# Optimization experiments

Hardware: AMD Instinct MI355X
Metric: run time of the kernel (lower is better)

The kernel has to match this reference:

```python
import jax, jax.numpy as jnp
import numpy as np

B, C, N, M_MODES, EMB = 8, 64, 2048, 32, 256
MFREQ = 2 * M_MODES * (2 * M_MODES - 1)  # 4032
SCALE = 1.0 / (C * C)


def setup_inputs() -> dict:
    key = jax.random.key(0)
    ks = jax.random.split(key, 16)
    d = {
        "x": jax.random.normal(ks[0], (B, C, N), jnp.float32),
        "emb": jax.random.normal(ks[1], (B, EMB), jnp.float32),
        "Vf_re": jax.random.normal(ks[2], (MFREQ, N), jnp.float32),
        "Vf_im": jax.random.normal(ks[3], (MFREQ, N), jnp.float32),
        "Vi_re": jax.random.normal(ks[4], (N, MFREQ), jnp.float32),
        "Vi_im": jax.random.normal(ks[5], (N, MFREQ), jnp.float32),
        "w1_re": SCALE * jax.random.uniform(ks[6], (C, C, M_MODES, M_MODES), jnp.float32),
        "w1_im": SCALE * jax.random.uniform(ks[7], (C, C, M_MODES, M_MODES), jnp.float32),
        "w2_re": SCALE * jax.random.uniform(ks[8], (C, C, M_MODES, M_MODES), jnp.float32),
        "w2_im": SCALE * jax.random.uniform(ks[9], (C, C, M_MODES, M_MODES), jnp.float32),
        "m1_re": SCALE * jax.random.uniform(ks[10], (1, M_MODES, M_MODES, EMB), jnp.float32),
        "m1_im": SCALE * jax.random.uniform(ks[11], (1, M_MODES, M_MODES, EMB), jnp.float32),
        "m2_re": SCALE * jax.random.uniform(ks[12], (1, M_MODES, M_MODES, EMB), jnp.float32),
        "m2_im": SCALE * jax.random.uniform(ks[13], (1, M_MODES, M_MODES, EMB), jnp.float32),
    }
    return d


def _spectral_conv(x, emb, Vf, Vi, w1, w2, mod1, mod2):
    m = M_MODES
    # nuft.forward: [B,N,C] complex -> [B,MFREQ,C]
    xc = jnp.transpose(x, (0, 2, 1)).astype(jnp.complex64)
    x_nfft = jnp.einsum('mn,bnc->bmc', Vf, xc)
    # [B,C,2m,2m-1]
    x_ft = jnp.transpose(x_nfft, (0, 2, 1)).reshape(x.shape[0], C, 2 * m, 2 * m - 1)
    embc = emb.astype(jnp.complex64)[:, None, None, :]  # [B,1,1,EMB]
    phi1 = jnp.sum(mod1 * embc, axis=-1)  # [B,m,m]
    phi2 = jnp.sum(mod2 * embc, axis=-1)
    out1 = jnp.einsum('bixy,ioxy->boxy', x_ft[:, :, :m, :m], w1)
    out2 = jnp.einsum('bixy,ioxy->boxy', x_ft[:, :, -m:, :m], w2)
    mod1b = phi1[:, None, :, :] * out1
    mod2b = phi2[:, None, :, :] * out2
    out_ft = jnp.concatenate([mod1b, mod2b], axis=2)  # [B,C,2m,m]
    xf = out_ft.reshape(x.shape[0], C, 2 * m * m)
    # Hermitian-symmetry reconstruction: flip over mode AND channel dims, conj
    xf2 = jnp.conj(jnp.flip(xf[..., 2 * m:], axis=(-2, -1)))
    xf = jnp.concatenate([xf, xf2], axis=-1)  # [B,C,MFREQ]
    xf = jnp.transpose(xf, (0, 2, 1))  # [B,MFREQ,C]
    out = jnp.einsum('nm,bmc->bnc', Vi, xf)  # nuft.inverse -> [B,N,C]
    out = jnp.transpose(out, (0, 2, 1)) / N * 2
    return out.real


def reference(x, emb, Vf_re, Vf_im, Vi_re, Vi_im, w1_re, w1_im, w2_re, w2_im, m1_re, m1_im, m2_re, m2_im):
    Vf = Vf_re + 1j * Vf_im
    Vi = Vi_re + 1j * Vi_im
    w1 = w1_re + 1j * w1_im
    w2 = w2_re + 1j * w2_im
    mod1 = m1_re + 1j * m1_im
    mod2 = m2_re + 1j * m2_im
    return _spectral_conv(x, emb, Vf, Vi, w1, w2, mod1, mod2)
```

## Files before the change

### kernel.cpp

```cpp
#include <hip/hip_runtime.h>

#define BB    8
#define CC    64
#define NN    2048
#define GG    2048
#define MFREQ 4032

typedef __attribute__((ext_vector_type(4))) float f32x4;
typedef __attribute__((ext_vector_type(8))) short bf16x8;

static __device__ __forceinline__ unsigned short f2bf(float f) {
    union { float f; unsigned u; } v; v.f = f;
    unsigned r = v.u + 0x7fff + ((v.u >> 16) & 1);
    return (unsigned short)(r >> 16);
}

#define ASYNC_COPY16(gp, lp)                                                        \
    __builtin_amdgcn_global_load_lds(                                               \
        (const __attribute__((address_space(1))) unsigned int*)(gp),                \
        (__attribute__((address_space(3))) unsigned int*)(lp), 16, 0, 0)

__global__ __launch_bounds__(256) void pack_all(const float* __restrict__ vf_re,
                                                const float* __restrict__ vf_im,
                                                const float* __restrict__ x,
                                                const float* __restrict__ vi_re,
                                                const float* __restrict__ vi_im,
                                                unsigned short* __restrict__ af,
                                                unsigned short* __restrict__ xb,
                                                unsigned short* __restrict__ mi) {
    int blk = blockIdx.x;
    float4 v;
    unsigned short* dst;
    if (blk < 8192) {
        int idx = blk * 256 + threadIdx.x;
        int m = idx >> 9;
        int q = (idx & 511) * 4;
        int g = m & 2047;
        int f = (g >> 5) * 63 + (g & 31);
        const float* src = (m < 2048 ? vf_re : vf_im) + (size_t)f * 2048 + q;
        v = *(const float4*)src;
        dst = af + (size_t)m * 2048 + q;
    } else if (blk < 9216) {
        int idx = (blk - 8192) * 256 + threadIdx.x;
        int q = idx * 4;
        v = *(const float4*)(x + q);
        dst = xb + q;
    } else {
        int idx = (blk - 9216) * 256 + threadIdx.x;
        int n = idx >> 11;
        int q4 = (idx & 2047) * 4;
        int region = q4 >> 11;
        int off = q4 & 2047;
        if (region == 0) {
            v = *(const float4*)(vi_re + (size_t)n * MFREQ + off);
        } else if (region == 1) {
            float4 t = *(const float4*)(vi_im + (size_t)n * MFREQ + off);
            v.x = -t.x; v.y = -t.y; v.z = -t.z; v.w = -t.w;
        } else {
            if (off < 64) { v.x = v.y = v.z = v.w = 0.0f; }
            else {
                const float* src = (region == 2 ? vi_re : vi_im);
                float4 t = *(const float4*)(src + (size_t)n * MFREQ + (4092 - off));
                v.x = t.w; v.y = t.z; v.z = t.y; v.w = t.x;
            }
        }
        dst = mi + (size_t)n * 8192 + q4;
    }
    ushort4 o; o.x = f2bf(v.x); o.y = f2bf(v.y); o.z = f2bf(v.z); o.w = f2bf(v.w);
    *(ushort4*)dst = o;
}

__global__ __launch_bounds__(256) void pack_wt(const float* __restrict__ w1_re,
                                               const float* __restrict__ w1_im,
                                               const float* __restrict__ w2_re,
                                               const float* __restrict__ w2_im,
                                               unsigned int* __restrict__ wt) {
    __shared__ float sre[64][65];
    __shared__ float sim[64][65];
    int wsel = blockIdx.z;
    const float* wre = wsel ? w2_re : w1_re;
    const float* wim = wsel ? w2_im : w1_im;
    int io0 = blockIdx.y * 64, xy0 = blockIdx.x * 64;
    int t = threadIdx.x;
    int r = t >> 2, cq = (t & 3) * 16;
    for (int j = 0; j < 16; j += 4) {
        float4 a = *(const float4*)(wre + (size_t)(io0 + r) * 1024 + xy0 + cq + j);
        float4 b = *(const float4*)(wim + (size_t)(io0 + r) * 1024 + xy0 + cq + j);
        sre[r][cq + j + 0] = a.x; sre[r][cq + j + 1] = a.y; sre[r][cq + j + 2] = a.z; sre[r][cq + j + 3] = a.w;
        sim[r][cq + j + 0] = b.x; sim[r][cq + j + 1] = b.y; sim[r][cq + j + 2] = b.z; sim[r][cq + j + 3] = b.w;
    }
    __syncthreads();
    int iol = t & 63, gq = t >> 6;
    for (int jj = 0; jj < 16; ++jj) {
        int gl = jj * 4 + gq;
        int g = xy0 + gl + wsel * 1024;
        unsigned int o = (unsigned int)f2bf(sre[iol][gl]) | ((unsigned int)f2bf(sim[iol][gl]) << 16);
        wt[(size_t)g * 4096 + io0 + iol] = o;
    }
}

__global__ __launch_bounds__(256) void phi_k(const float* __restrict__ m1_re,
                                             const float* __restrict__ m1_im,
                                             const float* __restrict__ m2_re,
                                             const float* __restrict__ m2_im,
                                             const float* __restrict__ emb,
                                             float* __restrict__ phi_re,
                                             float* __restrict__ phi_im) {
    int g = blockIdx.x, b = blockIdx.y, e = threadIdx.x;
    int xy = g & 1023;
    const float* mr = (g < 1024 ? m1_re : m2_re) + xy * 256;
    const float* mi = (g < 1024 ? m1_im : m2_im) + xy * 256;
    float em = emb[b * 256 + e];
    float pr = mr[e] * em, pi = mi[e] * em;
    __shared__ float sr[4], si[4];
    for (int s = 32; s > 0; s >>= 1) { pr += __shfl_down(pr, s); pi += __shfl_down(pi, s); }
    int wid = e >> 6;
    if ((e & 63) == 0) { sr[wid] = pr; si[wid] = pi; }
    __syncthreads();
    if (e == 0) {
        phi_re[b * 2048 + g] = sr[0] + sr[1] + sr[2] + sr[3];
        phi_im[b * 2048 + g] = si[0] + si[1] + si[2] + si[3];
    }
}

__global__ __launch_bounds__(256, 2) void gemm_sk(const unsigned short* __restrict__ A,
                                                  const unsigned short* __restrict__ Bm,
                                                  float* __restrict__ P,
                                                  int M, int N, int K, int Kper, int ilv) {
    __shared__ unsigned short As[128 * 64];
    __shared__ unsigned short Bs[128 * 64];
    int t = threadIdx.x;
    int lane = t & 63, w = t >> 6;
    int m0 = blockIdx.y * 128, n0 = blockIdx.x * 128;
    int z = blockIdx.z;
    int kbase = z * Kper;
    int wm = (w >> 1) * 64, wn = (w & 1) * 64;
    int lr = lane & 15, quad = lane >> 4;
    int rsub = lane >> 3, slot = lane & 7;

    f32x4 acc[4][4] = {};

    for (int kk = kbase; kk < kbase + Kper; kk += 64) {
        __syncthreads();
        #pragma unroll
        for (int l = 0; l < 4; ++l) {
            int r = (w * 4 + l) * 8 + rsub;
            int c = slot ^ (r & 7);
            ASYNC_COPY16(A + (size_t)(m0 + r) * K + kk + c * 8, As + r * 64 + slot * 8);
            ASYNC_COPY16(Bm + (size_t)(n0 + r) * K + kk + c * 8, Bs + r * 64 + slot * 8);
        }
        __syncthreads();
        #pragma unroll
        for (int ks = 0; ks < 2; ++ks) {
            bf16x8 af[4], bfr[4];
            #pragma unroll
            for (int i = 0; i < 4; ++i) {
                int row = wm + i * 16 + lr;
                int q = (ks * 4 + quad) ^ (row & 7);
                af[i] = *(const bf16x8*)(As + row * 64 + q * 8);
                int rowb = wn + i * 16 + lr;
                int qb = (ks * 4 + quad) ^ (rowb & 7);
                bfr[i] = *(const bf16x8*)(Bs + rowb * 64 + qb * 8);
            }
            #pragma unroll
            for (int i = 0; i < 4; ++i)
            #pragma unroll
            for (int j = 0; j < 4; ++j)
                acc[i][j] = __builtin_amdgcn_mfma_f32_16x16x32_bf16(af[i], bfr[j], acc[i][j], 0, 0, 0);
        }
    }
    float* Pz = P + (size_t)z * M * N;
    size_t rstride = ilv ? 1024 : (size_t)N;
    #pragma unroll
    for (int i = 0; i < 4; ++i)
    #pragma unroll
    for (int j = 0; j < 4; ++j) {
        int rr = m0 + wm + i * 16 + quad * 4;
        int cc = n0 + wn + j * 16 + lr;
        size_t base = ilv ? ((size_t)(rr & 2047) * 1024 + cc * 2 + (rr >> 11))
                          : ((size_t)rr * N + cc);
        float* cp = Pz + base;
        f32x4 v = acc[i][j];
        cp[0]           = v.x;
        cp[rstride]     = v.y;
        cp[2 * rstride] = v.z;
        cp[3 * rstride] = v.w;
    }
}

__global__ __launch_bounds__(256) void reduce_k(const float* __restrict__ P,
                                                float* __restrict__ out,
                                                int S, size_t elems, float alpha) {
    size_t idx = ((size_t)blockIdx.x * 256 + threadIdx.x) * 4;
    float4 s = *(const float4*)(P + idx);
    for (int zz = 1; zz < S; ++zz) {
        float4 v = *(const float4*)(P + (size_t)zz * elems + idx);
        s.x += v.x; s.y += v.y; s.z += v.z; s.w += v.w;
    }
    s.x *= alpha; s.y *= alpha; s.z *= alpha; s.w *= alpha;
    *(float4*)(out + idx) = s;
}

__global__ __launch_bounds__(256, 4) void middle_k(const float* __restrict__ O1,
                                                   const unsigned int* __restrict__ wt,
                                                   const float* __restrict__ phi_re,
                                                   const float* __restrict__ phi_im,
                                                   unsigned short* __restrict__ Yt) {
    __shared__ unsigned int sW[2][4096];
    __shared__ float sInc[2][1024];
    int t = threadIdx.x;
    int g0 = blockIdx.x * 2;
    int b = t >> 5, p = t & 31;

    #pragma unroll
    for (int gt = 0; gt < 2; ++gt) {
        int g = g0 + gt;
        #pragma unroll
        for (int j = 0; j < 4; ++j)
            ASYNC_COPY16(wt + (size_t)g * 4096 + (j * 256 + t) * 4, &sW[gt][(j * 256 + t) * 4]);
        ASYNC_COPY16(O1 + (size_t)g * 1024 + t * 4, &sInc[gt][t * 4]);
    }
    __syncthreads();

    unsigned short reA[2][2], imA[2][2];

    #pragma unroll
    for (int gt = 0; gt < 2; ++gt) {
        int g = g0 + gt;
        float ar0 = 0.f, ai0 = 0.f, ar1 = 0.f, ai1 = 0.f;
        const float2* incp = (const float2*)sInc[gt] + b * 64;
        const unsigned int* wp = sW[gt] + 2 * p;
        #pragma unroll 8
        for (int i = 0; i < 64; ++i) {
            float2 a = incp[i];
            uint2 uu = *(const uint2*)(wp + i * 64);
            float w0r = __uint_as_float(uu.x << 16);
            float w0i = __uint_as_float(uu.x & 0xffff0000u);
            float w1r = __uint_as_float(uu.y << 16);
            float w1i = __uint_as_float(uu.y & 0xffff0000u);
            ar0 += a.x * w0r - a.y * w0i;  ai0 += a.x * w0i + a.y * w0r;
            ar1 += a.x * w1r - a.y * w1i;  ai1 += a.x * w1i + a.y * w1r;
        }
        float pr = phi_re[b * 2048 + g], pi = phi_im[b * 2048 + g];
        reA[0][gt] = f2bf(pr * ar0 - pi * ai0);
        imA[0][gt] = f2bf(pr * ai0 + pi * ar0);
        reA[1][gt] = f2bf(pr * ar1 - pi * ai1);
        imA[1][gt] = f2bf(pr * ai1 + pi * ar1);
    }

    #pragma unroll
    for (int ch = 0; ch < 2; ++ch) {
        int c = 2 * p + ch;
        size_t r0 = (size_t)(b * 64 + c) * 8192;
        size_t rf = (size_t)(b * 64 + 63 - c) * 8192;
        unsigned int ure = (unsigned int)reA[ch][0] | ((unsigned int)reA[ch][1] << 16);
        unsigned int uim = (unsigned int)imA[ch][0] | ((unsigned int)imA[ch][1] << 16);
        *(unsigned int*)(Yt + r0 + g0)        = ure;
        *(unsigned int*)(Yt + r0 + 2048 + g0) = uim;
        *(unsigned int*)(Yt + rf + 4096 + g0) = ure;
        *(unsigned int*)(Yt + rf + 6144 + g0) = uim;
    }
}

extern "C" void kernel_launch(void* const* d_in, const int* in_sizes, int n_in,
                              void* d_out, int out_size, void* d_ws, size_t ws_size,
                              hipStream_t stream) {
    const float* x     = (const float*)d_in[0];
    const float* emb   = (const float*)d_in[1];
    const float* vf_re = (const float*)d_in[2];
    const float* vf_im = (const float*)d_in[3];
    const float* vi_re = (const float*)d_in[4];
    const float* vi_im = (const float*)d_in[5];
    const float* w1_re = (const float*)d_in[6];
    const float* w1_im = (const float*)d_in[7];
    const float* w2_re = (const float*)d_in[8];
    const float* w2_im = (const float*)d_in[9];
    const float* m1_re = (const float*)d_in[10];
    const float* m1_im = (const float*)d_in[11];
    const float* m2_re = (const float*)d_in[12];
    const float* m2_im = (const float*)d_in[13];

    char* ws = (char*)d_ws;
    unsigned short* Af = (unsigned short*)(ws);
    unsigned short* Xb = (unsigned short*)(ws + 16777216);
    unsigned short* Mi = (unsigned short*)(ws + 18874368);
    unsigned int*   Wt = (unsigned int*)(ws + 52428800);
    float*          O1 = (float*)(ws + 85983232);
    float*       PhiRe = (float*)(ws + 94371840);
    float*       PhiIm = (float*)(ws + 94437376);
    unsigned short* Yt = (unsigned short*)(ws + 94502912);
    float*          P  = (float*)(ws + 102891520);
    float* out = (float*)d_out;

    pack_all<<<25600, 256, 0, stream>>>(vf_re, vf_im, x, vi_re, vi_im, Af, Xb, Mi);
    pack_wt<<<dim3(16, 64, 2), 256, 0, stream>>>(w1_re, w1_im, w2_re, w2_im, Wt);
    phi_k<<<dim3(2048, 8), 256, 0, stream>>>(m1_re, m1_im, m2_re, m2_im, emb, PhiRe, PhiIm);

    gemm_sk<<<dim3(4, 32, 4), 256, 0, stream>>>(Af, Xb, P, 4096, 512, 2048, 512, 1);
    reduce_k<<<2048, 256, 0, stream>>>(P, O1, 4, (size_t)4096 * 512, 1.0f);

    middle_k<<<1024, 256, 0, stream>>>(O1, Wt, PhiRe, PhiIm, Yt);

    gemm_sk<<<dim3(16, 4, 8), 256, 0, stream>>>(Yt, Mi, P, 512, 2048, 8192, 1024, 0);
    reduce_k<<<1024, 256, 0, stream>>>(P, out, 8, (size_t)512 * 2048, 1.0f / 1024.0f);
}
```

Baseline: 330.9 us.

## Fuse split-K reduction into middle kernel and coarsen pack and phi kernels

Removes the separate reduce pass after the forward GEMM by summing the four split-K partials directly inside middle_k while loading its input tile, which drops one launch and one round trip of O1 through memory. pack_all now handles four float4 elements per thread, so it launches a quarter as many blocks. phi_k loads each modulation row once and loops over the batch inside the block instead of using one block per batch entry. The costs are a synchronous load of the partials in middle_k in place of the async copy, and extra __syncthreads in phi_k.

```diff
diff --git a/kernel.cpp b/kernel.cpp
--- a/kernel.cpp
+++ b/kernel.cpp
@@ -29,45 +29,59 @@
                                                 unsigned short* __restrict__ xb,
                                                 unsigned short* __restrict__ mi) {
     int blk = blockIdx.x;
-    float4 v;
-    unsigned short* dst;
-    if (blk < 8192) {
-        int idx = blk * 256 + threadIdx.x;
-        int m = idx >> 9;
-        int q = (idx & 511) * 4;
-        int g = m & 2047;
-        int f = (g >> 5) * 63 + (g & 31);
-        const float* src = (m < 2048 ? vf_re : vf_im) + (size_t)f * 2048 + q;
-        v = *(const float4*)src;
-        dst = af + (size_t)m * 2048 + q;
-    } else if (blk < 9216) {
-        int idx = (blk - 8192) * 256 + threadIdx.x;
-        int q = idx * 4;
-        v = *(const float4*)(x + q);
-        dst = xb + q;
+    int t = threadIdx.x;
+    float4 v[4];
+    unsigned short* dst[4];
+    if (blk < 2048) {
+        #pragma unroll
+        for (int u = 0; u < 4; ++u) {
+            int idx = blk * 1024 + u * 256 + t;
+            int m = idx >> 9;
+            int q = (idx & 511) * 4;
+            int g = m & 2047;
+            int f = (g >> 5) * 63 + (g & 31);
+            const float* src = (m < 2048 ? vf_re : vf_im) + (size_t)f * 2048 + q;
+            v[u] = *(const float4*)src;
+            dst[u] = af + (size_t)m * 2048 + q;
+        }
+    } else if (blk < 2304) {
+        #pragma unroll
+        for (int u = 0; u < 4; ++u) {
+            int idx = (blk - 2048) * 1024 + u * 256 + t;
+            int q = idx * 4;
+            v[u] = *(const float4*)(x + q);
+            dst[u] = xb + q;
+        }
     } else {
-        int idx = (blk - 9216) * 256 + threadIdx.x;
-        int n = idx >> 11;
-        int q4 = (idx & 2047) * 4;
-        int region = q4 >> 11;
-        int off = q4 & 2047;
-        if (region == 0) {
-            v = *(const float4*)(vi_re + (size_t)n * MFREQ + off);
-        } else if (region == 1) {
-            float4 t = *(const float4*)(vi_im + (size_t)n * MFREQ + off);
-            v.x = -t.x; v.y = -t.y; v.z = -t.z; v.w = -t.w;
-        } else {
-            if (off < 64) { v.x = v.y = v.z = v.w = 0.0f; }
-            else {
-                const float* src = (region == 2 ? vi_re : vi_im);
-                float4 t = *(const float4*)(src + (size_t)n * MFREQ + (4092 - off));
-                v.x = t.w; v.y = t.z; v.z = t.y; v.w = t.x;
+        #pragma unroll
+        for (int u = 0; u < 4; ++u) {
+            int idx = (blk - 2304) * 1024 + u * 256 + t;
+            int n = idx >> 11;
+            int q4 = (idx & 2047) * 4;
+            int region = q4 >> 11;
+            int off = q4 & 2047;
+            if (region == 0) {
+                v[u] = *(const float4*)(vi_re + (size_t)n * MFREQ + off);
+            } else if (region == 1) {
+                float4 tt = *(const float4*)(vi_im + (size_t)n * MFREQ + off);
+                v[u].x = -tt.x; v[u].y = -tt.y; v[u].z = -tt.z; v[u].w = -tt.w;
+            } else {
+                if (off < 64) { v[u].x = v[u].y = v[u].z = v[u].w = 0.0f; }
+                else {
+                    const float* src = (region == 2 ? vi_re : vi_im);
+                    float4 tt = *(const float4*)(src + (size_t)n * MFREQ + (4092 - off));
+                    v[u].x = tt.w; v[u].y = tt.z; v[u].z = tt.y; v[u].w = tt.x;
+                }
             }
-        }
-        dst = mi + (size_t)n * 8192 + q4;
-    }
-    ushort4 o; o.x = f2bf(v.x); o.y = f2bf(v.y); o.z = f2bf(v.z); o.w = f2bf(v.w);
-    *(ushort4*)dst = o;
+            dst[u] = mi + (size_t)n * 8192 + q4;
+        }
+    }
+    #pragma unroll
+    for (int u = 0; u < 4; ++u) {
+        ushort4 o;
+        o.x = f2bf(v[u].x); o.y = f2bf(v[u].y); o.z = f2bf(v[u].z); o.w = f2bf(v[u].w);
+        *(ushort4*)dst[u] = o;
+    }
 }
 
 __global__ __launch_bounds__(256) void pack_wt(const float* __restrict__ w1_re,
@@ -106,20 +120,24 @@
                                              const float* __restrict__ emb,
                                              float* __restrict__ phi_re,
                                              float* __restrict__ phi_im) {
-    int g = blockIdx.x, b = blockIdx.y, e = threadIdx.x;
+    int g = blockIdx.x, e = threadIdx.x;
     int xy = g & 1023;
     const float* mr = (g < 1024 ? m1_re : m2_re) + xy * 256;
     const float* mi = (g < 1024 ? m1_im : m2_im) + xy * 256;
-    float em = emb[b * 256 + e];
-    float pr = mr[e] * em, pi = mi[e] * em;
+    float vr = mr[e], vi = mi[e];
     __shared__ float sr[4], si[4];
-    for (int s = 32; s > 0; s >>= 1) { pr += __shfl_down(pr, s); pi += __shfl_down(pi, s); }
-    int wid = e >> 6;
-    if ((e & 63) == 0) { sr[wid] = pr; si[wid] = pi; }
-    __syncthreads();
-    if (e == 0) {
-        phi_re[b * 2048 + g] = sr[0] + sr[1] + sr[2] + sr[3];
-        phi_im[b * 2048 + g] = si[0] + si[1] + si[2] + si[3];
+    for (int bb = 0; bb < 8; ++bb) {
+        float em = emb[bb * 256 + e];
+        float pr = vr * em, pi = vi * em;
+        for (int s = 32; s > 0; s >>= 1) { pr += __shfl_down(pr, s); pi += __shfl_down(pi, s); }
+        int wid = e >> 6;
+        if ((e & 63) == 0) { sr[wid] = pr; si[wid] = pi; }
+        __syncthreads();
+        if (e == 0) {
+            phi_re[bb * 2048 + g] = sr[0] + sr[1] + sr[2] + sr[3];
+            phi_im[bb * 2048 + g] = si[0] + si[1] + si[2] + si[3];
+        }
+        __syncthreads();
     }
 }
 
@@ -201,7 +219,7 @@
     *(float4*)(out + idx) = s;
 }
 
-__global__ __launch_bounds__(256, 4) void middle_k(const float* __restrict__ O1,
+__global__ __launch_bounds__(256, 4) void middle_k(const float* __restrict__ P,
                                                    const unsigned int* __restrict__ wt,
                                                    const float* __restrict__ phi_re,
                                                    const float* __restrict__ phi_im,
@@ -218,7 +236,13 @@
         #pragma unroll
         for (int j = 0; j < 4; ++j)
             ASYNC_COPY16(wt + (size_t)g * 4096 + (j * 256 + t) * 4, &sW[gt][(j * 256 + t) * 4]);
-        ASYNC_COPY16(O1 + (size_t)g * 1024 + t * 4, &sInc[gt][t * 4]);
+        float4 s = *(const float4*)(P + (size_t)g * 1024 + t * 4);
+        #pragma unroll
+        for (int z = 1; z < 4; ++z) {
+            float4 pv = *(const float4*)(P + (size_t)z * 2097152 + (size_t)g * 1024 + t * 4);
+            s.x += pv.x; s.y += pv.y; s.z += pv.z; s.w += pv.w;
+        }
+        *(float4*)(&sInc[gt][t * 4]) = s;
     }
     __syncthreads();
 
@@ -285,21 +309,19 @@
     unsigned short* Xb = (unsigned short*)(ws + 16777216);
     unsigned short* Mi = (unsigned short*)(ws + 18874368);
     unsigned int*   Wt = (unsigned int*)(ws + 52428800);
-    float*          O1 = (float*)(ws + 85983232);
     float*       PhiRe = (float*)(ws + 94371840);
     float*       PhiIm = (float*)(ws + 94437376);
     unsigned short* Yt = (unsigned short*)(ws + 94502912);
     float*          P  = (float*)(ws + 102891520);
     float* out = (float*)d_out;
 
-    pack_all<<<25600, 256, 0, stream>>>(vf_re, vf_im, x, vi_re, vi_im, Af, Xb, Mi);
+    pack_all<<<6400, 256, 0, stream>>>(vf_re, vf_im, x, vi_re, vi_im, Af, Xb, Mi);
     pack_wt<<<dim3(16, 64, 2), 256, 0, stream>>>(w1_re, w1_im, w2_re, w2_im, Wt);
-    phi_k<<<dim3(2048, 8), 256, 0, stream>>>(m1_re, m1_im, m2_re, m2_im, emb, PhiRe, PhiIm);
+    phi_k<<<2048, 256, 0, stream>>>(m1_re, m1_im, m2_re, m2_im, emb, PhiRe, PhiIm);
 
     gemm_sk<<<dim3(4, 32, 4), 256, 0, stream>>>(Af, Xb, P, 4096, 512, 2048, 512, 1);
-    reduce_k<<<2048, 256, 0, stream>>>(P, O1, 4, (size_t)4096 * 512, 1.0f);
-
-    middle_k<<<1024, 256, 0, stream>>>(O1, Wt, PhiRe, PhiIm, Yt);
+
+    middle_k<<<1024, 256, 0, stream>>>(P, Wt, PhiRe, PhiIm, Yt);
 
     gemm_sk<<<dim3(16, 4, 8), 256, 0, stream>>>(Yt, Mi, P, 512, 2048, 8192, 1024, 0);
     reduce_k<<<1024, 256, 0, stream>>>(P, out, 8, (size_t)512 * 2048, 1.0f / 1024.0f);
```

Measured after the change: 316.5 us. 1.05x faster.
